# Optimization experiments

Measured on AMD Instinct MI355X. Metric: run time of the kernel, lower is better.

The kernel has to match this reference:

```python
import jax, jax.numpy as jnp
import numpy as np

B, C, H, W = 8, 192, 64, 64
HEADS = 4


def _conv(x, w, groups=1):
    # NCHW conv, stride 1, SAME padding (matches 1x1 pad=0 and 3x3 pad=1)
    return jax.lax.conv_general_dilated(
        x, w, window_strides=(1, 1), padding='SAME',
        dimension_numbers=('NCHW', 'OIHW', 'NCHW'),
        feature_group_count=groups)


def setup_inputs() -> dict:
    key = jax.random.key(0)
    k1, k2, k3, k4 = jax.random.split(key, 4)
    x = jax.random.normal(k1, (B, C, H, W), dtype=jnp.float32)
    y = jax.random.normal(k2, (B, C, H, W), dtype=jnp.float32)
    # qkv: Conv2d(C, 3C, 1, bias=False) -> weight (3C, C, 1, 1)
    w_qkv = jax.random.normal(k3, (3 * C, C, 1, 1), dtype=jnp.float32) * 0.02
    # qkv_conv: depthwise Conv2d(3C, 3C, 3, padding=1, groups=3C) -> weight (3C, 1, 3, 3)
    w_dw = jax.random.normal(k4, (3 * C, 1, 3, 3), dtype=jnp.float32) * 0.1
    temperature = jnp.ones((1, HEADS, 1, 1), dtype=jnp.float32)
    return {'x': x, 'y': y, 'w_qkv': w_qkv, 'w_dw': w_dw, 'temperature': temperature}


def reference(x, y, w_qkv, w_dw, temperature):
    b, c, h, w = x.shape
    hw = h * w
    dh = c // HEADS

    def qkv(t):
        t = _conv(_conv(t, w_qkv), w_dw, groups=3 * c)  # (b, 3c, h, w)
        q, k, v = jnp.split(t, 3, axis=1)
        rs = lambda a: a.reshape(b, HEADS, dh, hw)
        return rs(q), rs(k), rs(v)

    q, k, v = qkv(x)
    q1, k1, v1 = qkv(y)

    # F.normalize along last dim (eps = 1e-12)
    def nrm(a):
        n = jnp.sqrt(jnp.sum(a * a, axis=-1, keepdims=True))
        return a / jnp.maximum(n, 1e-12)

    q, k, q1, k1 = nrm(q), nrm(k), nrm(q1), nrm(k1)

    # channel attention: (b, heads, dh, dh), temperature broadcasts (1, heads, 1, 1)
    attn = lambda a, bk: jax.nn.softmax(
        jnp.einsum('bhcn,bhdn->bhcd', a, bk) * temperature, axis=-1)

    attn_u = attn(q, k)
    attn_ud = attn(q, k1)
    attn_d = attn(q1, k1)
    attn_du = attn(q1, k)

    mm = lambda A, V: jnp.einsum('bhcd,bhdn->bhcn', A, V)
    cross_feature = (mm(attn_du, v) + mm(attn_ud, v1)).reshape(b, c, h, w)
    self_feature = (mm(attn_u, v) + mm(attn_d, v1)).reshape(b, c, h, w)
    return cross_feature, self_feature
```

## Files before the change

kernel.cpp:

```cpp
#include <hip/hip_runtime.h>

#define CC   192
#define C3   576
#define HH   64
#define WW   64
#define HWP  4096
#define BB   8
#define DH   48
#define QKV_B (C3*HWP)
#define X_B   (CC*HWP)
#define OUT_HALF ((size_t)BB*X_B)

typedef short bf16x8 __attribute__((ext_vector_type(8)));
typedef float f32x4  __attribute__((ext_vector_type(4)));

#define AS1(p) ((__attribute__((address_space(1))) void*)(p))
#define AS3(p) ((__attribute__((address_space(3))) void*)(p))

__device__ __forceinline__ ushort f2bf(float v) {
    union { float f; unsigned u; } a; a.f = v;
    unsigned r = a.u + 0x7FFF + ((a.u >> 16) & 1);
    return (ushort)(r >> 16);
}
__device__ __forceinline__ float bf2f(ushort h) {
    union { float f; unsigned u; } a; a.u = ((unsigned)h) << 16; return a.f;
}

__global__ __launch_bounds__(256) void convert_single_kernel(const float* __restrict__ x,
    const float* __restrict__ y, ushort* __restrict__ xt)
{
    __shared__ float L[64][65];
    const int n0 = blockIdx.x * 64, c0 = blockIdx.y * 64, z = blockIdx.z;
    const int t = threadIdx.x;
    const float* ip = ((z < 8) ? x : y) + (size_t)(z & 7) * X_B;
    #pragma unroll
    for (int i = 0; i < 16; i++) {
        int e = t + 256 * i;
        int r = e >> 6, col = e & 63;
        L[r][col] = ip[(size_t)(c0 + r) * HWP + n0 + col];
    }
    __syncthreads();
    #pragma unroll
    for (int i = 0; i < 4; i++) {
        int e = t + 256 * i;
        int n = e >> 4, c4 = e & 15;
        ushort hi[4];
        #pragma unroll
        for (int j = 0; j < 4; j++)
            hi[j] = f2bf(L[c4 * 4 + j][n]);
        size_t base = ((size_t)z * HWP + n0 + n) * 192 + c0 + c4 * 4;
        *(ushort4*)&xt[base] = make_ushort4(hi[0], hi[1], hi[2], hi[3]);
    }
}

__global__ __launch_bounds__(256) void vtrans_kernel(const ushort* __restrict__ in,
    ushort* __restrict__ vt)
{
    __shared__ __align__(16) ushort L[64][72];
    const int n0 = blockIdx.x * 64, c0 = blockIdx.y * 64, z = blockIdx.z;
    const int t = threadIdx.x;
    const ushort* ip = in + (size_t)z * X_B;
    #pragma unroll
    for (int i = 0; i < 2; i++) {
        int e = t + 256 * i;
        int r = e >> 3, u8 = e & 7;
        *(bf16x8*)&L[r][u8 * 8] = *(const bf16x8*)&ip[(size_t)(c0 + r) * HWP + n0 + u8 * 8];
    }
    __syncthreads();
    #pragma unroll
    for (int i = 0; i < 4; i++) {
        int e = t + 256 * i;
        int n = e >> 4, c4 = e & 15;
        ushort o[4];
        #pragma unroll
        for (int j = 0; j < 4; j++) o[j] = L[c4 * 4 + j][n];
        *(ushort4*)&vt[((size_t)z * HWP + n0 + n) * 192 + c0 + c4 * 4] =
            make_ushort4(o[0], o[1], o[2], o[3]);
    }
}

__global__ __launch_bounds__(256) void wconvert_kernel(const float* __restrict__ wq,
    ushort* __restrict__ wc)
{
    int e = (blockIdx.x * 256 + threadIdx.x) * 4;
    int oc = e / 192, k = e % 192;
    ushort o[4] = {0, 0, 0, 0};
    if (oc < C3) {
        #pragma unroll
        for (int j = 0; j < 4; j++)
            o[j] = f2bf(wq[oc * CC + k + j]);
    }
    *(ushort4*)&wc[e] = make_ushort4(o[0], o[1], o[2], o[3]);
}

__global__ __launch_bounds__(512) void conv1x1_mfma(const ushort* __restrict__ XT,
    const ushort* __restrict__ Wc, ushort* __restrict__ t1s)
{
    __shared__ __align__(16) ushort Wsb[2][128 * 32];
    __shared__ __align__(16) ushort Xsb[2][256 * 32];
    const int t = threadIdx.x;
    const int lane = t & 63, w = t >> 6;
    const int wm = w >> 2, wn = w & 3;
    const int fr = lane & 15, kg = lane >> 4;
    const int g = blockIdx.x;
    const int xcd = g & 7, s = g >> 3;
    const int bg = xcd;
    const int tsr = s / 80;
    const int rem = s - tsr * 80;
    const int nt = rem / 5;
    const int mi = rem % 5;
    const int n0 = nt * 256;
    const int m0 = mi * 128;
    const ushort* XTp = XT + (size_t)(tsr * 8 + bg) * (HWP * 192);

    f32x4 acc[4][4] = {};

    auto STAGE = [&](int buf, int ck) {
        const int k0 = ck * 32;
        {
            int u = t;
            int rp = u >> 3;
            int p = (u & 7) ^ (rp & 7);
            int r = (rp << 1) | (p >> 2);
            int c = p & 3;
            const ushort* gw = Wc + (size_t)(m0 + r) * 192 + k0 + c * 8;
            __builtin_amdgcn_global_load_lds(AS1(gw), AS3(&Wsb[buf][(size_t)t * 8]), 16, 0, 0);
        }
        #pragma unroll
        for (int i = 0; i < 2; i++) {
            int u = i * 512 + t;
            int rp = u >> 3;
            int p = (u & 7) ^ (rp & 7);
            int r = (rp << 1) | (p >> 2);
            int c = p & 3;
            const ushort* gx = XTp + (size_t)(n0 + r) * 192 + k0 + c * 8;
            __builtin_amdgcn_global_load_lds(AS1(gx), AS3(&Xsb[buf][(size_t)(i * 512 + t) * 8]), 16, 0, 0);
        }
    };

    STAGE(0, 0);
    __syncthreads();
    int cur = 0;
    for (int ck = 0; ck < 6; ck++) {
        if (ck < 5) STAGE(cur ^ 1, ck + 1);
        bf16x8 afh[4], bfr[4];
        #pragma unroll
        for (int m = 0; m < 4; m++) {
            int R = wm * 64 + m * 16 + fr;
            int unit = (R >> 1) * 8 + ((((R & 1) << 2) | kg) ^ ((R >> 1) & 7));
            afh[m] = *(const bf16x8*)&Wsb[cur][unit * 8];
        }
        #pragma unroll
        for (int n = 0; n < 4; n++) {
            int R = wn * 64 + n * 16 + fr;
            int unit = (R >> 1) * 8 + ((((R & 1) << 2) | kg) ^ ((R >> 1) & 7));
            bfr[n] = *(const bf16x8*)&Xsb[cur][unit * 8];
        }
        #pragma unroll
        for (int m = 0; m < 4; m++)
            #pragma unroll
            for (int n = 0; n < 4; n++)
                acc[m][n] = __builtin_amdgcn_mfma_f32_16x16x32_bf16(afh[m], bfr[n], acc[m][n], 0, 0, 0);
        __syncthreads();
        cur ^= 1;
    }

    ushort (*E)[128] = (ushort(*)[128])Xsb;
    ushort* ob = t1s + (size_t)tsr * ((size_t)BB * QKV_B) + (size_t)bg * QKV_B;
    #pragma unroll
    for (int hf = 0; hf < 2; hf++) {
        if (hf) __syncthreads();
        if ((wn >> 1) == hf) {
            int wn2 = wn & 1;
            #pragma unroll
            for (int m = 0; m < 4; m++) {
                int rl = wm * 64 + m * 16 + kg * 4;
                #pragma unroll
                for (int n = 0; n < 4; n++) {
                    int cl = wn2 * 64 + n * 16 + fr;
                    #pragma unroll
                    for (int r = 0; r < 4; r++)
                        E[rl + r][cl] = f2bf(acc[m][n][r]);
                }
            }
        }
        __syncthreads();
        #pragma unroll
        for (int i = 0; i < 4; i++) {
            int u = t + 512 * i;
            int row = u >> 4, c8 = u & 15;
            int oc = m0 + row;
            if (oc < C3)
                *(bf16x8*)&ob[(size_t)oc * HWP + n0 + hf * 128 + c8 * 8] =
                    *(bf16x8*)&E[row][c8 * 8];
        }
    }
}

__global__ __launch_bounds__(256) void dw3x3_kernel(const ushort* __restrict__ inp,
    const float* __restrict__ wd,
    ushort* __restrict__ qh0, ushort* __restrict__ vv0, float* __restrict__ inv0)
{
    __shared__ float P[66][76];
    const int bcg = blockIdx.x;
    const int tsr = bcg / (BB * C3);
    const int bc = bcg - tsr * (BB * C3);
    const int b = bc / C3, ch = bc % C3;
    const int t = threadIdx.x;
    const ushort* ip = inp + (size_t)tsr * ((size_t)BB * QKV_B) + (size_t)bc * HWP;
    ushort* qh = qh0 + (size_t)tsr * 12582912;
    ushort* vv = vv0 + (size_t)tsr * 6291456;
    float* inv = inv0 + (size_t)tsr * 3072;
    float wr[9];
    #pragma unroll
    for (int k = 0; k < 9; k++) wr[k] = wd[ch * 9 + k];
    for (int i = t; i < 66 * 76; i += 256) ((float*)P)[i] = 0.f;
    __syncthreads();
    #pragma unroll
    for (int i = 0; i < 2; i++) {
        int u = t + 256 * i;
        int y = u >> 3, x0 = (u & 7) * 8;
        bf16x8 v8 = *(const bf16x8*)&ip[u * 8];
        float f0 = bf2f((ushort)v8[0]), f1 = bf2f((ushort)v8[1]);
        float f2 = bf2f((ushort)v8[2]), f3 = bf2f((ushort)v8[3]);
        float f4 = bf2f((ushort)v8[4]), f5 = bf2f((ushort)v8[5]);
        float f6 = bf2f((ushort)v8[6]), f7 = bf2f((ushort)v8[7]);
        *(float4*)&P[1 + y][4 + x0]     = make_float4(f0, f1, f2, f3);
        *(float4*)&P[1 + y][4 + x0 + 4] = make_float4(f4, f5, f6, f7);
    }
    __syncthreads();

    const int tx = t & 15, ty = t >> 4;
    const int x0 = tx * 4, y0 = ty * 4;

    float ssum = 0.f;
    float4 a0 = *(float4*)&P[y0][x0], b0 = *(float4*)&P[y0][x0 + 4], c0 = *(float4*)&P[y0][x0 + 8];
    float4 a1 = *(float4*)&P[y0 + 1][x0], b1 = *(float4*)&P[y0 + 1][x0 + 4], c1 = *(float4*)&P[y0 + 1][x0 + 8];
    #pragma unroll
    for (int r = 0; r < 4; r++) {
        float4 a2 = *(float4*)&P[y0 + r + 2][x0];
        float4 b2 = *(float4*)&P[y0 + r + 2][x0 + 4];
        float4 c2 = *(float4*)&P[y0 + r + 2][x0 + 8];
        float res[4] = {0.f, 0.f, 0.f, 0.f};
        {
            float e0 = a0.w, e1 = b0.x, e2 = b0.y, e3 = b0.z, e4 = b0.w, e5 = c0.x;
            res[0] += wr[0]*e0 + wr[1]*e1 + wr[2]*e2;
            res[1] += wr[0]*e1 + wr[1]*e2 + wr[2]*e3;
            res[2] += wr[0]*e2 + wr[1]*e3 + wr[2]*e4;
            res[3] += wr[0]*e3 + wr[1]*e4 + wr[2]*e5;
        }
        {
            float e0 = a1.w, e1 = b1.x, e2 = b1.y, e3 = b1.z, e4 = b1.w, e5 = c1.x;
            res[0] += wr[3]*e0 + wr[4]*e1 + wr[5]*e2;
            res[1] += wr[3]*e1 + wr[4]*e2 + wr[5]*e3;
            res[2] += wr[3]*e2 + wr[4]*e3 + wr[5]*e4;
            res[3] += wr[3]*e3 + wr[4]*e4 + wr[5]*e5;
        }
        {
            float e0 = a2.w, e1 = b2.x, e2 = b2.y, e3 = b2.z, e4 = b2.w, e5 = c2.x;
            res[0] += wr[6]*e0 + wr[7]*e1 + wr[8]*e2;
            res[1] += wr[6]*e1 + wr[7]*e2 + wr[8]*e3;
            res[2] += wr[6]*e2 + wr[7]*e3 + wr[8]*e4;
            res[3] += wr[6]*e3 + wr[7]*e4 + wr[8]*e5;
        }
        #pragma unroll
        for (int k = 0; k < 4; k++) ssum += res[k] * res[k];
        int px = (y0 + r) * WW + x0;
        if (ch < 384) {
            size_t base = ((size_t)b * 384 + ch) * HWP + px;
            *(ushort4*)&qh[base] = make_ushort4(f2bf(res[0]), f2bf(res[1]),
                                                f2bf(res[2]), f2bf(res[3]));
        } else {
            size_t base = ((size_t)b * CC + (ch - 384)) * HWP + px;
            *(ushort4*)&vv[base] = make_ushort4(f2bf(res[0]), f2bf(res[1]),
                                                f2bf(res[2]), f2bf(res[3]));
        }
        a0 = a1; b0 = b1; c0 = c1;
        a1 = a2; b1 = b2; c1 = c2;
    }
    if (ch < 384) {
        #pragma unroll
        for (int off = 32; off > 0; off >>= 1) ssum += __shfl_down(ssum, off);
        __shared__ float red[4];
        if ((t & 63) == 0) red[t >> 6] = ssum;
        __syncthreads();
        if (t == 0) {
            float tot = red[0] + red[1] + red[2] + red[3];
            inv[b * 384 + ch] = 1.f / fmaxf(sqrtf(tot), 1e-12f);
        }
    }
}

__global__ __launch_bounds__(256) void gram_mfma(const ushort* __restrict__ qhx,
    const ushort* __restrict__ qhy, float* __restrict__ spart)
{
    __shared__ __align__(16) ushort As[96 * 64];
    __shared__ __align__(16) ushort Bs[96 * 64];
    const int chunk = blockIdx.x, bh = blockIdx.y;
    const int b = bh >> 2, h = bh & 3;
    const int t = threadIdx.x;
    const int lane = t & 63, w = t >> 6;
    const int wm = w >> 1, wn = w & 1;
    const int fr = lane & 15, kg = lane >> 4;

    const size_t qbase = ((size_t)b * 384 + h * DH) * HWP;
    const size_t kbase = ((size_t)b * 384 + 192 + h * DH) * HWP;

    f32x4 acc[3][3] = {};

    for (int ks = 0; ks < 8; ks++) {
        const int n0 = chunk * 512 + ks * 64;
        #pragma unroll
        for (int i = 0; i < 3; i++) {
            int u = i * 256 + w * 64 + lane;
            int r = u >> 3, c = u & 7;
            int cs = c ^ (r & 7);
            const ushort* ga = ((r < DH) ? (qhx + qbase + (size_t)r * HWP)
                                         : (qhy + qbase + (size_t)(r - DH) * HWP))
                               + n0 + cs * 8;
            __builtin_amdgcn_global_load_lds(AS1(ga), AS3(&As[(size_t)(i * 4 + w) * 512]), 16, 0, 0);
            const ushort* gb = ((r < DH) ? (qhx + kbase + (size_t)r * HWP)
                                         : (qhy + kbase + (size_t)(r - DH) * HWP))
                               + n0 + cs * 8;
            __builtin_amdgcn_global_load_lds(AS1(gb), AS3(&Bs[(size_t)(i * 4 + w) * 512]), 16, 0, 0);
        }
        __syncthreads();
        #pragma unroll
        for (int kq = 0; kq < 8; kq += 4) {
            bf16x8 af[3], bfr[3];
            #pragma unroll
            for (int m = 0; m < 3; m++) {
                int R = wm * DH + m * 16 + fr;
                int unit = R * 8 + ((kq + kg) ^ (R & 7));
                af[m] = *(const bf16x8*)&As[unit * 8];
            }
            #pragma unroll
            for (int n = 0; n < 3; n++) {
                int R = wn * DH + n * 16 + fr;
                int unit = R * 8 + ((kq + kg) ^ (R & 7));
                bfr[n] = *(const bf16x8*)&Bs[unit * 8];
            }
            #pragma unroll
            for (int m = 0; m < 3; m++)
                #pragma unroll
                for (int n = 0; n < 3; n++)
                    acc[m][n] = __builtin_amdgcn_mfma_f32_16x16x32_bf16(af[m], bfr[n], acc[m][n], 0, 0, 0);
        }
        __syncthreads();
    }

    float* sp = spart + ((size_t)chunk * 32 + bh) * 9216;
    #pragma unroll
    for (int m = 0; m < 3; m++) {
        int row = wm * DH + m * 16 + kg * 4;
        #pragma unroll
        for (int n = 0; n < 3; n++) {
            int col = wn * DH + n * 16 + fr;
            #pragma unroll
            for (int r = 0; r < 4; r++)
                sp[(row + r) * 96 + col] = acc[m][n][r];
        }
    }
}

__global__ __launch_bounds__(256) void softmax_kernel(const float* __restrict__ spart,
    const float* __restrict__ invx, const float* __restrict__ invy,
    const float* __restrict__ temp, ushort* __restrict__ mpp)
{
    __shared__ float G[96][97];
    const int bh = blockIdx.x, b = bh >> 2, h = bh & 3;
    const int t = threadIdx.x;
    const float ts = temp[h];
    for (int i = 0; i < 36; i++) {
        int f = t + 256 * i;
        float s = 0.f;
        #pragma unroll
        for (int cch = 0; cch < 8; cch++)
            s += spart[((size_t)cch * 32 + bh) * 9216 + f];
        int r = f / 96, c = f % 96;
        float iq = (r < DH) ? invx[b*384 + h*DH + r] : invy[b*384 + h*DH + (r-DH)];
        float ik = (c < DH) ? invx[b*384 + CC + h*DH + c] : invy[b*384 + CC + h*DH + (c-DH)];
        G[r][c] = s * iq * ik * ts;
    }
    __syncthreads();
    if (t < 192) {
        int r = t >> 1, hf = t & 1;
        float* rowp = &G[r][hf * DH];
        float m = rowp[0];
        for (int i = 1; i < DH; i++) m = fmaxf(m, rowp[i]);
        float s = 0.f;
        for (int i = 0; i < DH; i++) { float e = __expf(rowp[i] - m); rowp[i] = e; s += e; }
        float inv = 1.f / s;
        for (int i = 0; i < DH; i++) rowp[i] *= inv;
    }
    __syncthreads();
    ushort* mo = mpp + (size_t)bh * 96 * 128;
    for (int i = 0; i < 12; i++) {
        int f = t + 256 * i;
        int r = f / 32, p = f % 32;
        int ch = p >> 4, j = p & 15;
        mo[(size_t)r * 128 + ch * 64 + 48 + j] = 0;
    }
    for (int i = 0; i < 36; i++) {
        int f = t + 256 * i;
        int r = f / 96, c = f % 96;
        float v;
        if (c < DH) v = (r < DH) ? G[DH + r][c] : G[r - DH][c];
        else        v = G[r][c];
        ushort hi = f2bf(v);
        if (c < DH) mo[(size_t)r * 128 + c] = hi;
        else        mo[(size_t)r * 128 + 64 + (c - DH)] = hi;
    }
}

__global__ __launch_bounds__(256) void outmm_mfma(const ushort* __restrict__ VTx,
    const ushort* __restrict__ VTy, const ushort* __restrict__ mpp,
    float* __restrict__ out)
{
    __shared__ __align__(16) ushort As[96 * 64];
    __shared__ __align__(16) ushort Bs[128 * 64];
    const int t = threadIdx.x;
    const int lane = t & 63, w = t >> 6;
    const int wm = w >> 1, wn = w & 1;
    const int fr = lane & 15, kg = lane >> 4;
    const int nc = blockIdx.x, bh = blockIdx.y;
    const int b = bh >> 2, h = bh & 3;
    const int n0 = nc * 128;
    const ushort* mp = mpp + (size_t)bh * 96 * 128;

    f32x4 acc[3][4] = {};

    for (int kc = 0; kc < 2; kc++) {
        const ushort* Vsrc = kc ? VTy : VTx;
        const int coff = h * DH;
        const int aoff = kc * 64;
        #pragma unroll
        for (int i = 0; i < 3; i++) {
            int u = i * 256 + w * 64 + lane;
            int r = u >> 3, c = u & 7;
            int cs = c ^ (r & 7);
            const ushort* ga = mp + (size_t)r * 128 + aoff + cs * 8;
            __builtin_amdgcn_global_load_lds(AS1(ga), AS3(&As[(size_t)(i * 4 + w) * 512]), 16, 0, 0);
        }
        #pragma unroll
        for (int i = 0; i < 4; i++) {
            int u = i * 256 + w * 64 + lane;
            int r = u >> 3, c = u & 7;
            int cs = c ^ (r & 7);
            int c8 = coff + cs * 8;
            if (c8 >= 192) c8 -= 192;
            const ushort* gb = Vsrc + ((size_t)(b * HWP + n0 + r)) * 192 + c8;
            __builtin_amdgcn_global_load_lds(AS1(gb), AS3(&Bs[(size_t)(i * 4 + w) * 512]), 16, 0, 0);
        }
        __syncthreads();
        #pragma unroll
        for (int kq = 0; kq < 8; kq += 4) {
            bf16x8 af[3], bfr[4];
            #pragma unroll
            for (int m = 0; m < 3; m++) {
                int R = wm * DH + m * 16 + fr;
                int unit = R * 8 + ((kq + kg) ^ (R & 7));
                af[m] = *(const bf16x8*)&As[unit * 8];
            }
            #pragma unroll
            for (int n = 0; n < 4; n++) {
                int R = wn * 64 + n * 16 + fr;
                int unit = R * 8 + ((kq + kg) ^ (R & 7));
                bfr[n] = *(const bf16x8*)&Bs[unit * 8];
            }
            #pragma unroll
            for (int m = 0; m < 3; m++)
                #pragma unroll
                for (int n = 0; n < 4; n++)
                    acc[m][n] = __builtin_amdgcn_mfma_f32_16x16x32_bf16(af[m], bfr[n], acc[m][n], 0, 0, 0);
        }
        __syncthreads();
    }

    #pragma unroll
    for (int m = 0; m < 3; m++) {
        int row = wm * DH + m * 16 + kg * 4;
        #pragma unroll
        for (int n = 0; n < 4; n++) {
            int col = n0 + wn * 64 + n * 16 + fr;
            #pragma unroll
            for (int r = 0; r < 4; r++) {
                int rr = row + r;
                float* dst = (rr < DH)
                    ? (out + (size_t)b * X_B + (h * DH + rr) * HWP + col)
                    : (out + OUT_HALF + (size_t)b * X_B + (h * DH + rr - DH) * HWP + col);
                *dst = acc[m][n][r];
            }
        }
    }
}

extern "C" void kernel_launch(void* const* d_in, const int* in_sizes, int n_in,
                              void* d_out, int out_size, void* d_ws, size_t ws_size,
                              hipStream_t stream)
{
    const float* x  = (const float*)d_in[0];
    const float* y  = (const float*)d_in[1];
    const float* wq = (const float*)d_in[2];
    const float* wd = (const float*)d_in[3];
    const float* tp = (const float*)d_in[4];
    float* out = (float*)d_out;
    float* ws = (float*)d_ws;

    ushort* qh0 = (ushort*)ws;
    float*  v0f = ws + 12582912;
    ushort* v0  = (ushort*)v0f;
    float*  t10 = ws + 12582912 + 6291456;
    ushort* t1s = (ushort*)t10;
    ushort* XT  = (ushort*)(ws + 12582912 + 6291456 + 18874368);
    ushort* Wc  = (ushort*)(ws + 12582912 + 6291456 + 18874368 + 6291456);
    float*  inv0 = ws + 12582912 + 6291456 + 18874368 + 6291456 + 61440;
    float*  invx = inv0;
    float*  invy = inv0 + 3072;
    ushort* VTx  = t1s;
    ushort* VTy  = (ushort*)(t10 + 3145728);
    float*  spart = t10 + 6291456;
    ushort* Mpp  = (ushort*)(t10 + 6291456 + 2359296);
    ushort* qhx = qh0;
    ushort* qhy = qh0 + 12582912;

    wconvert_kernel<<<120, 256, 0, stream>>>(wq, Wc);

    convert_single_kernel<<<dim3(64, 3, 16), 256, 0, stream>>>(x, y, XT);
    conv1x1_mfma<<<1280, 512, 0, stream>>>(XT, Wc, t1s);
    dw3x3_kernel<<<2 * BB * C3, 256, 0, stream>>>(t1s, wd, qh0, v0, inv0);

    vtrans_kernel<<<dim3(64, 3, 16), 256, 0, stream>>>(v0, VTx);

    gram_mfma<<<dim3(8, 32), 256, 0, stream>>>(qhx, qhy, spart);
    softmax_kernel<<<32, 256, 0, stream>>>(spart, invx, invy, tp, Mpp);
    outmm_mfma<<<dim3(HWP / 128, 32), 256, 0, stream>>>(VTx, VTy, Mpp, out);
}
```

Before: 142.4 us.

## Keep X tile resident in LDS and loop over all output-channel tiles per block

The 1x1 conv GEMM now loads the full 256-pixel by 192-channel X tile into LDS once per block and loops over the five 128-row weight tiles, streaming only weights through a double buffer. The grid drops from 1280 to 256 blocks, so each X tile is read from global memory once instead of five times. The cost is less parallelism (256 blocks of 512 threads, one wave per CU on a 256-CU part), larger LDS use (about 136 KB), and an X preload that does not overlap with compute.

```diff
diff --git a/kernel.cpp b/kernel.cpp
--- a/kernel.cpp
+++ b/kernel.cpp
@@ -96,36 +96,24 @@
 __global__ __launch_bounds__(512) void conv1x1_mfma(const ushort* __restrict__ XT,
     const ushort* __restrict__ Wc, ushort* __restrict__ t1s)
 {
-    __shared__ __align__(16) ushort Wsb[2][128 * 32];
-    __shared__ __align__(16) ushort Xsb[2][256 * 32];
+    __shared__ __align__(16) ushort Xres[6][1024 * 8];
+    __shared__ __align__(16) ushort Wsb[2][512 * 8];
+    __shared__ __align__(16) ushort E[128][128];
     const int t = threadIdx.x;
     const int lane = t & 63, w = t >> 6;
     const int wm = w >> 2, wn = w & 3;
     const int fr = lane & 15, kg = lane >> 4;
     const int g = blockIdx.x;
-    const int xcd = g & 7, s = g >> 3;
-    const int bg = xcd;
-    const int tsr = s / 80;
-    const int rem = s - tsr * 80;
-    const int nt = rem / 5;
-    const int mi = rem % 5;
+    const int bg = g & 7, s = g >> 3;
+    const int tsr = s >> 4;
+    const int nt = s & 15;
     const int n0 = nt * 256;
-    const int m0 = mi * 128;
     const ushort* XTp = XT + (size_t)(tsr * 8 + bg) * (HWP * 192);
-
-    f32x4 acc[4][4] = {};
-
-    auto STAGE = [&](int buf, int ck) {
+    ushort* ob = t1s + (size_t)(tsr * 8 + bg) * QKV_B;
+
+    #pragma unroll
+    for (int ck = 0; ck < 6; ck++) {
         const int k0 = ck * 32;
-        {
-            int u = t;
-            int rp = u >> 3;
-            int p = (u & 7) ^ (rp & 7);
-            int r = (rp << 1) | (p >> 2);
-            int c = p & 3;
-            const ushort* gw = Wc + (size_t)(m0 + r) * 192 + k0 + c * 8;
-            __builtin_amdgcn_global_load_lds(AS1(gw), AS3(&Wsb[buf][(size_t)t * 8]), 16, 0, 0);
-        }
         #pragma unroll
         for (int i = 0; i < 2; i++) {
             int u = i * 512 + t;
@@ -134,66 +122,85 @@
             int r = (rp << 1) | (p >> 2);
             int c = p & 3;
             const ushort* gx = XTp + (size_t)(n0 + r) * 192 + k0 + c * 8;
-            __builtin_amdgcn_global_load_lds(AS1(gx), AS3(&Xsb[buf][(size_t)(i * 512 + t) * 8]), 16, 0, 0);
-        }
+            __builtin_amdgcn_global_load_lds(AS1(gx), AS3(&Xres[ck][(size_t)(i * 512 + t) * 8]), 16, 0, 0);
+        }
+    }
+
+    auto STAGE_W = [&](int buf, int mi, int ck) {
+        const int k0 = ck * 32;
+        int u = t;
+        int rp = u >> 3;
+        int p = (u & 7) ^ (rp & 7);
+        int r = (rp << 1) | (p >> 2);
+        int c = p & 3;
+        const ushort* gw = Wc + (size_t)(mi * 128 + r) * 192 + k0 + c * 8;
+        __builtin_amdgcn_global_load_lds(AS1(gw), AS3(&Wsb[buf][(size_t)t * 8]), 16, 0, 0);
     };
 
-    STAGE(0, 0);
+    STAGE_W(0, 0, 0);
     __syncthreads();
     int cur = 0;
-    for (int ck = 0; ck < 6; ck++) {
-        if (ck < 5) STAGE(cur ^ 1, ck + 1);
-        bf16x8 afh[4], bfr[4];
-        #pragma unroll
-        for (int m = 0; m < 4; m++) {
-            int R = wm * 64 + m * 16 + fr;
-            int unit = (R >> 1) * 8 + ((((R & 1) << 2) | kg) ^ ((R >> 1) & 7));
-            afh[m] = *(const bf16x8*)&Wsb[cur][unit * 8];
-        }
-        #pragma unroll
-        for (int n = 0; n < 4; n++) {
-            int R = wn * 64 + n * 16 + fr;
-            int unit = (R >> 1) * 8 + ((((R & 1) << 2) | kg) ^ ((R >> 1) & 7));
-            bfr[n] = *(const bf16x8*)&Xsb[cur][unit * 8];
-        }
-        #pragma unroll
-        for (int m = 0; m < 4; m++)
-            #pragma unroll
-            for (int n = 0; n < 4; n++)
-                acc[m][n] = __builtin_amdgcn_mfma_f32_16x16x32_bf16(afh[m], bfr[n], acc[m][n], 0, 0, 0);
+
+    for (int mi = 0; mi < 5; mi++) {
+        f32x4 acc[4][4] = {};
+        for (int ck = 0; ck < 6; ck++) {
+            if (mi * 6 + ck < 29) {
+                int nmi = (ck == 5) ? mi + 1 : mi;
+                int nck = (ck == 5) ? 0 : ck + 1;
+                STAGE_W(cur ^ 1, nmi, nck);
+            }
+            bf16x8 afh[4], bfr[4];
+            #pragma unroll
+            for (int m = 0; m < 4; m++) {
+                int R = wm * 64 + m * 16 + fr;
+                int unit = (R >> 1) * 8 + ((((R & 1) << 2) | kg) ^ ((R >> 1) & 7));
+                afh[m] = *(const bf16x8*)&Wsb[cur][unit * 8];
+            }
+            #pragma unroll
+            for (int n = 0; n < 4; n++) {
+                int R = wn * 64 + n * 16 + fr;
+                int unit = (R >> 1) * 8 + ((((R & 1) << 2) | kg) ^ ((R >> 1) & 7));
+                bfr[n] = *(const bf16x8*)&Xres[ck][unit * 8];
+            }
+            #pragma unroll
+            for (int m = 0; m < 4; m++)
+                #pragma unroll
+                for (int n = 0; n < 4; n++)
+                    acc[m][n] = __builtin_amdgcn_mfma_f32_16x16x32_bf16(afh[m], bfr[n], acc[m][n], 0, 0, 0);
+            __syncthreads();
+            cur ^= 1;
+        }
+
+        const int m0 = mi * 128;
+        #pragma unroll
+        for (int hf = 0; hf < 2; hf++) {
+            if (hf) __syncthreads();
+            if ((wn >> 1) == hf) {
+                int wn2 = wn & 1;
+                #pragma unroll
+                for (int m = 0; m < 4; m++) {
+                    int rl = wm * 64 + m * 16 + kg * 4;
+                    #pragma unroll
+                    for (int n = 0; n < 4; n++) {
+                        int cl = wn2 * 64 + n * 16 + fr;
+                        #pragma unroll
+                        for (int r = 0; r < 4; r++)
+                            E[rl + r][cl] = f2bf(acc[m][n][r]);
+                    }
+                }
+            }
+            __syncthreads();
+            #pragma unroll
+            for (int i = 0; i < 4; i++) {
+                int u = t + 512 * i;
+                int row = u >> 4, c8 = u & 15;
+                int oc = m0 + row;
+                if (oc < C3)
+                    *(bf16x8*)&ob[(size_t)oc * HWP + n0 + hf * 128 + c8 * 8] =
+                        *(bf16x8*)&E[row][c8 * 8];
+            }
+        }
         __syncthreads();
-        cur ^= 1;
-    }
-
-    ushort (*E)[128] = (ushort(*)[128])Xsb;
-    ushort* ob = t1s + (size_t)tsr * ((size_t)BB * QKV_B) + (size_t)bg * QKV_B;
-    #pragma unroll
-    for (int hf = 0; hf < 2; hf++) {
-        if (hf) __syncthreads();
-        if ((wn >> 1) == hf) {
-            int wn2 = wn & 1;
-            #pragma unroll
-            for (int m = 0; m < 4; m++) {
-                int rl = wm * 64 + m * 16 + kg * 4;
-                #pragma unroll
-                for (int n = 0; n < 4; n++) {
-                    int cl = wn2 * 64 + n * 16 + fr;
-                    #pragma unroll
-                    for (int r = 0; r < 4; r++)
-                        E[rl + r][cl] = f2bf(acc[m][n][r]);
-                }
-            }
-        }
-        __syncthreads();
-        #pragma unroll
-        for (int i = 0; i < 4; i++) {
-            int u = t + 512 * i;
-            int row = u >> 4, c8 = u & 15;
-            int oc = m0 + row;
-            if (oc < C3)
-                *(bf16x8*)&ob[(size_t)oc * HWP + n0 + hf * 128 + c8 * 8] =
-                    *(bf16x8*)&E[row][c8 * 8];
-        }
     }
 }
 
@@ -527,7 +534,7 @@
     wconvert_kernel<<<120, 256, 0, stream>>>(wq, Wc);
 
     convert_single_kernel<<<dim3(64, 3, 16), 256, 0, stream>>>(x, y, XT);
-    conv1x1_mfma<<<1280, 512, 0, stream>>>(XT, Wc, t1s);
+    conv1x1_mfma<<<256, 512, 0, stream>>>(XT, Wc, t1s);
     dw3x3_kernel<<<2 * BB * C3, 256, 0, stream>>>(t1s, wd, qh0, v0, inv0);
 
     vtrans_kernel<<<dim3(64, 3, 16), 256, 0, stream>>>(v0, VTx);
```

Result: faster. 138.9 us (median of 2 runs) (-2.4%).
